# Performance work log

Measured on AMD Instinct MI355X. Metric: run time of the kernel, lower is better.

## Reference

```python
import jax, jax.numpy as jnp
import numpy as np

NUM_HEADS = 4
HEAD_DIM = 64  # out_dim // num_heads = 256 // 4
NEG_SLOPE = 0.2


def setup_inputs() -> dict:
    key = jax.random.key(0)
    k1, k2 = jax.random.split(key)
    h = jax.random.normal(k1, (8, 2048, 256), dtype=jnp.float32)
    # Linear(in_dim, head_dim*num_heads, bias=False): store as [in_dim, out_dim]
    W = jax.random.normal(k2, (256, 256), dtype=jnp.float32) * (1.0 / np.sqrt(256.0))
    return {"h": h, "W": W}


def reference(h, W):
    B, T, _ = h.shape
    # Wh: (B, H, T, D)
    Wh = (h @ W).reshape(B, T, NUM_HEADS, HEAD_DIM).transpose(0, 2, 1, 3)
    scale = 1.0 / (HEAD_DIM ** 0.5)
    # full T x T scores per head, LeakyReLU then softmax over keys
    scores = jnp.einsum('bhtd,bhsd->bhts', Wh, Wh) * scale
    attention = jax.nn.softmax(jax.nn.leaky_relu(scores, negative_slope=NEG_SLOPE), axis=-1)
    h_prime = jnp.einsum('bhts,bhsd->bhtd', attention, Wh)
    # concat=True: (B, T, H*D)
    return h_prime.transpose(0, 2, 1, 3).reshape(B, T, NUM_HEADS * HEAD_DIM)
```

## Files before the change

kernel.cpp:

```cpp
#include <hip/hip_runtime.h>

#define T_SEQ 2048
#define NH 4
#define DH 64

typedef __bf16 bf16x8 __attribute__((ext_vector_type(8)));
typedef float f32x4 __attribute__((ext_vector_type(4)));

__device__ __forceinline__ unsigned short f2bf_rne(float x) {
  unsigned int u = __builtin_bit_cast(unsigned int, x);
  u += 0x7fffu + ((u >> 16) & 1u);
  return (unsigned short)(u >> 16);
}

__device__ __forceinline__ void async_cp16(const unsigned short* g, unsigned short* l) {
  __builtin_amdgcn_global_load_lds(
      (const __attribute__((address_space(1))) unsigned int*)g,
      (__attribute__((address_space(3))) unsigned int*)l, 16, 0, 0);
}

__global__ __launch_bounds__(256, 2) void wh_gemm(
    const float* __restrict__ h, const float* __restrict__ W,
    unsigned short* __restrict__ Kb, unsigned short* __restrict__ Vt) {
  __shared__ __align__(16) float hs[32 * 256];
  const int tid = threadIdx.x;
  const int mbase = blockIdx.x * 32;
  const float4* hblk = (const float4*)(h + (size_t)mbase * 256);
#pragma unroll
  for (int i = 0; i < 8; i++) {
    int slot = i * 256 + tid;
    ((float4*)hs)[slot] = hblk[slot];
  }
  __syncthreads();
  const int nid = tid & 63;
  const int rg = tid >> 6;
  float acc[8][4];
#pragma unroll
  for (int r = 0; r < 8; r++)
#pragma unroll
    for (int j = 0; j < 4; j++) acc[r][j] = 0.f;
  const float4* Wv = (const float4*)W;
  for (int k = 0; k < 256; k += 2) {
    float4 w0 = Wv[k * 64 + nid];
    float4 w1 = Wv[(k + 1) * 64 + nid];
#pragma unroll
    for (int r = 0; r < 8; r++) {
      float2 hv = *(const float2*)&hs[(rg * 8 + r) * 256 + k];
      acc[r][0] += hv.x * w0.x; acc[r][1] += hv.x * w0.y;
      acc[r][2] += hv.x * w0.z; acc[r][3] += hv.x * w0.w;
      acc[r][0] += hv.y * w1.x; acc[r][1] += hv.y * w1.y;
      acc[r][2] += hv.y * w1.z; acc[r][3] += hv.y * w1.w;
    }
  }
  const float s1 = 0.424664717f;
  const int head = nid >> 4;
  const int d0 = (nid & 15) * 4;
#pragma unroll
  for (int r = 0; r < 8; r++) {
    int m = mbase + rg * 8 + r;
    int b = m >> 11, t = m & 2047;
    size_t bh = (size_t)(b * NH + head);
    ushort4 kp;
    kp.x = f2bf_rne(acc[r][0] * s1);
    kp.y = f2bf_rne(acc[r][1] * s1);
    kp.z = f2bf_rne(acc[r][2] * s1);
    kp.w = f2bf_rne(acc[r][3] * s1);
    *(ushort4*)&Kb[(bh * T_SEQ + t) * DH + d0] = kp;
    size_t vtb = (bh * DH + d0) * T_SEQ + t;
    Vt[vtb]             = f2bf_rne(acc[r][0]);
    Vt[vtb + T_SEQ]     = f2bf_rne(acc[r][1]);
    Vt[vtb + 2 * T_SEQ] = f2bf_rne(acc[r][2]);
    Vt[vtb + 3 * T_SEQ] = f2bf_rne(acc[r][3]);
  }
}

__global__ __launch_bounds__(256, 4) void attn(
    const unsigned short* __restrict__ Kb, const unsigned short* __restrict__ Vt,
    float* __restrict__ out) {
  __shared__ __align__(16) unsigned short ldsK[64 * 64];
  __shared__ __align__(16) unsigned short ldsV[64 * 64];
  __shared__ __align__(16) unsigned short ldsP[4][16 * 64];
  const int tid = threadIdx.x;
  const int wave = tid >> 6;
  const int lane = tid & 63;
  const int l15 = lane & 15;
  const int quad = lane >> 4;
  const int bh = blockIdx.x >> 5;
  const int qtile = blockIdx.x & 31;
  const unsigned short* Kbh = Kb + (size_t)bh * T_SEQ * DH;
  const unsigned short* Vbh = Vt + (size_t)bh * DH * T_SEQ;

  const int qrow = qtile * 64 + wave * 16 + l15;
  bf16x8 aq0 = *(const bf16x8*)&Kbh[qrow * DH + quad * 8];
  bf16x8 aq1 = *(const bf16x8*)&Kbh[qrow * DH + 32 + quad * 8];

  f32x4 o[4];
  float lsum[4];
#pragma unroll
  for (int i = 0; i < 4; i++) {
    o[i] = (f32x4){0.f, 0.f, 0.f, 0.f};
    lsum[i] = 0.f;
  }
  unsigned short* Pw = ldsP[wave];

  for (int kt = 0; kt < 32; kt++) {
    __syncthreads();
#pragma unroll
    for (int i = 0; i < 2; i++) {
      int slot = i * 256 + tid;
      int r = slot >> 3;
      int c = (slot & 7) ^ (r & 7);
      unsigned short* lb = &ldsK[(i * 256 + wave * 64) * 8];
      async_cp16(&Kbh[(kt * 64 + r) * DH + c * 8], lb);
      unsigned short* lbv = &ldsV[(i * 256 + wave * 64) * 8];
      async_cp16(&Vbh[(size_t)r * T_SEQ + kt * 64 + c * 8], lbv);
    }
    __syncthreads();

    f32x4 sfr[4];
#pragma unroll
    for (int nt = 0; nt < 4; nt++) {
      int key = nt * 16 + l15;
      bf16x8 kf0 = *(const bf16x8*)&ldsK[key * 64 + ((quad ^ (key & 7)) << 3)];
      bf16x8 kf1 = *(const bf16x8*)&ldsK[key * 64 + (((4 + quad) ^ (key & 7)) << 3)];
      f32x4 s = {0.f, 0.f, 0.f, 0.f};
      s = __builtin_amdgcn_mfma_f32_16x16x32_bf16(aq0, kf0, s, 0, 0, 0);
      s = __builtin_amdgcn_mfma_f32_16x16x32_bf16(aq1, kf1, s, 0, 0, 0);
      sfr[nt] = s;
    }

#pragma unroll
    for (int nt = 0; nt < 4; nt++) {
      int col = nt * 16 + l15;
#pragma unroll
      for (int reg = 0; reg < 4; reg++) {
        float v = sfr[nt][reg];
        float e = __builtin_amdgcn_exp2f(fmaxf(v, 0.2f * v));
        lsum[reg] += e;
        int row = quad * 4 + reg;
        Pw[(row << 6) + (((((col >> 3) ^ (row & 7))) << 3) | (col & 7))] =
            (unsigned short)(__builtin_bit_cast(unsigned int, e) >> 16);
      }
    }
    __builtin_amdgcn_s_waitcnt(0xC07F);

#pragma unroll
    for (int kc = 0; kc < 2; kc++) {
      bf16x8 ap = *(const bf16x8*)&Pw[(l15 << 6) + ((((kc << 2) + quad) ^ (l15 & 7)) << 3)];
#pragma unroll
      for (int nt = 0; nt < 4; nt++) {
        int d = nt * 16 + l15;
        bf16x8 vf = *(const bf16x8*)&ldsV[(d << 6) + ((((kc << 2) + quad) ^ (d & 7)) << 3)];
        o[nt] = __builtin_amdgcn_mfma_f32_16x16x32_bf16(ap, vf, o[nt], 0, 0, 0);
      }
    }
  }

  float inv[4];
#pragma unroll
  for (int reg = 0; reg < 4; reg++) {
    float l = lsum[reg];
    l += __shfl_xor(l, 1, 64);
    l += __shfl_xor(l, 2, 64);
    l += __shfl_xor(l, 4, 64);
    l += __shfl_xor(l, 8, 64);
    inv[reg] = 1.0f / l;
  }
  const int b = bh >> 2, head = bh & 3;
#pragma unroll
  for (int nt = 0; nt < 4; nt++) {
    int d = nt * 16 + l15;
#pragma unroll
    for (int reg = 0; reg < 4; reg++) {
      int trow = qtile * 64 + wave * 16 + quad * 4 + reg;
      out[((size_t)b * T_SEQ + trow) * 256 + head * 64 + d] = o[nt][reg] * inv[reg];
    }
  }
}

extern "C" void kernel_launch(void* const* d_in, const int* in_sizes, int n_in,
                              void* d_out, int out_size, void* d_ws, size_t ws_size,
                              hipStream_t stream) {
  const float* h = (const float*)d_in[0];
  const float* W = (const float*)d_in[1];
  float* out = (float*)d_out;
  unsigned short* Kb = (unsigned short*)d_ws;
  unsigned short* Vt = Kb + (size_t)32 * T_SEQ * DH;
  wh_gemm<<<512, 256, 0, stream>>>(h, W, Kb, Vt);
  attn<<<32 * 32, 256, 0, stream>>>(Kb, Vt, out);
}
```

Baseline: 161.3 us.

## Use split-bf16 MFMA for projection GEMM and double-buffer attention K/V tiles

The fp32 FMA projection GEMM is replaced with bf16 MFMA using a hi/lo split (three MFMAs per tile) to keep near-fp32 accuracy. A new prep kernel transposes W into split bf16 form. The attention kernel now double-buffers K/V LDS tiles with async prefetch of the next tile, raises wave priority around the MFMA sections, and remaps block IDs across XCDs for L2 locality. This adds an extra kernel launch and doubles LDS use, which may reduce occupancy.

```diff
diff --git a/kernel.cpp b/kernel.cpp
--- a/kernel.cpp
+++ b/kernel.cpp
@@ -6,6 +6,7 @@
 
 typedef __bf16 bf16x8 __attribute__((ext_vector_type(8)));
 typedef float f32x4 __attribute__((ext_vector_type(4)));
+typedef unsigned short u16x8 __attribute__((ext_vector_type(8)));
 
 __device__ __forceinline__ unsigned short f2bf_rne(float x) {
   unsigned int u = __builtin_bit_cast(unsigned int, x);
@@ -19,74 +20,107 @@
       (__attribute__((address_space(3))) unsigned int*)l, 16, 0, 0);
 }
 
+__global__ __launch_bounds__(256) void wprep(const float* __restrict__ W,
+                                             unsigned short* __restrict__ Wt) {
+  int tid = blockIdx.x * 256 + threadIdx.x;
+  int k = tid >> 8, n = tid & 255;
+  float w = W[tid];
+  unsigned int u = __builtin_bit_cast(unsigned int, w);
+  unsigned short hi = (unsigned short)(u >> 16);
+  float fhi = __builtin_bit_cast(float, u & 0xffff0000u);
+  float lo = w - fhi;
+  Wt[n * 256 + k] = hi;
+  Wt[65536 + n * 256 + k] =
+      (unsigned short)(__builtin_bit_cast(unsigned int, lo) >> 16);
+}
+
 __global__ __launch_bounds__(256, 2) void wh_gemm(
-    const float* __restrict__ h, const float* __restrict__ W,
+    const float* __restrict__ h, const unsigned short* __restrict__ Wt,
     unsigned short* __restrict__ Kb, unsigned short* __restrict__ Vt) {
-  __shared__ __align__(16) float hs[32 * 256];
   const int tid = threadIdx.x;
+  const int wave = tid >> 6;
+  const int lane = tid & 63;
+  const int l15 = lane & 15;
+  const int quad = lane >> 4;
   const int mbase = blockIdx.x * 32;
-  const float4* hblk = (const float4*)(h + (size_t)mbase * 256);
-#pragma unroll
-  for (int i = 0; i < 8; i++) {
-    int slot = i * 256 + tid;
-    ((float4*)hs)[slot] = hblk[slot];
-  }
-  __syncthreads();
-  const int nid = tid & 63;
-  const int rg = tid >> 6;
-  float acc[8][4];
-#pragma unroll
-  for (int r = 0; r < 8; r++)
-#pragma unroll
-    for (int j = 0; j < 4; j++) acc[r][j] = 0.f;
-  const float4* Wv = (const float4*)W;
-  for (int k = 0; k < 256; k += 2) {
-    float4 w0 = Wv[k * 64 + nid];
-    float4 w1 = Wv[(k + 1) * 64 + nid];
-#pragma unroll
-    for (int r = 0; r < 8; r++) {
-      float2 hv = *(const float2*)&hs[(rg * 8 + r) * 256 + k];
-      acc[r][0] += hv.x * w0.x; acc[r][1] += hv.x * w0.y;
-      acc[r][2] += hv.x * w0.z; acc[r][3] += hv.x * w0.w;
-      acc[r][0] += hv.y * w1.x; acc[r][1] += hv.y * w1.y;
-      acc[r][2] += hv.y * w1.z; acc[r][3] += hv.y * w1.w;
-    }
-  }
+  const int col0 = wave * 64;
+
+  f32x4 acc[2][4];
+#pragma unroll
+  for (int mt = 0; mt < 2; mt++)
+#pragma unroll
+    for (int nt = 0; nt < 4; nt++) acc[mt][nt] = (f32x4){0.f, 0.f, 0.f, 0.f};
+
+  for (int ks = 0; ks < 8; ks++) {
+    const int k0 = ks * 32 + quad * 8;
+    bf16x8 ahi[2], alo[2];
+#pragma unroll
+    for (int mt = 0; mt < 2; mt++) {
+      const float* hp = h + (size_t)(mbase + mt * 16 + l15) * 256 + k0;
+      float xf[8];
+      *(float4*)&xf[0] = *(const float4*)hp;
+      *(float4*)&xf[4] = *(const float4*)(hp + 4);
+      u16x8 hh, ll;
+#pragma unroll
+      for (int j = 0; j < 8; j++) {
+        unsigned int u = __builtin_bit_cast(unsigned int, xf[j]);
+        hh[j] = (unsigned short)(u >> 16);
+        float lo = xf[j] - __builtin_bit_cast(float, u & 0xffff0000u);
+        ll[j] = (unsigned short)(__builtin_bit_cast(unsigned int, lo) >> 16);
+      }
+      ahi[mt] = __builtin_bit_cast(bf16x8, hh);
+      alo[mt] = __builtin_bit_cast(bf16x8, ll);
+    }
+#pragma unroll
+    for (int nt = 0; nt < 4; nt++) {
+      const unsigned short* wp = Wt + ((size_t)(col0 + nt * 16 + l15) << 8) + k0;
+      bf16x8 bhi = *(const bf16x8*)wp;
+      bf16x8 blo = *(const bf16x8*)(wp + 65536);
+#pragma unroll
+      for (int mt = 0; mt < 2; mt++) {
+        acc[mt][nt] = __builtin_amdgcn_mfma_f32_16x16x32_bf16(ahi[mt], bhi, acc[mt][nt], 0, 0, 0);
+        acc[mt][nt] = __builtin_amdgcn_mfma_f32_16x16x32_bf16(alo[mt], bhi, acc[mt][nt], 0, 0, 0);
+        acc[mt][nt] = __builtin_amdgcn_mfma_f32_16x16x32_bf16(ahi[mt], blo, acc[mt][nt], 0, 0, 0);
+      }
+    }
+  }
+
   const float s1 = 0.424664717f;
-  const int head = nid >> 4;
-  const int d0 = (nid & 15) * 4;
-#pragma unroll
-  for (int r = 0; r < 8; r++) {
-    int m = mbase + rg * 8 + r;
-    int b = m >> 11, t = m & 2047;
-    size_t bh = (size_t)(b * NH + head);
-    ushort4 kp;
-    kp.x = f2bf_rne(acc[r][0] * s1);
-    kp.y = f2bf_rne(acc[r][1] * s1);
-    kp.z = f2bf_rne(acc[r][2] * s1);
-    kp.w = f2bf_rne(acc[r][3] * s1);
-    *(ushort4*)&Kb[(bh * T_SEQ + t) * DH + d0] = kp;
-    size_t vtb = (bh * DH + d0) * T_SEQ + t;
-    Vt[vtb]             = f2bf_rne(acc[r][0]);
-    Vt[vtb + T_SEQ]     = f2bf_rne(acc[r][1]);
-    Vt[vtb + 2 * T_SEQ] = f2bf_rne(acc[r][2]);
-    Vt[vtb + 3 * T_SEQ] = f2bf_rne(acc[r][3]);
+#pragma unroll
+  for (int mt = 0; mt < 2; mt++) {
+    int row = mbase + mt * 16 + quad * 4;
+    int b = row >> 11;
+    int tb = row & 2047;
+    size_t bh = (size_t)(b * NH + wave);
+#pragma unroll
+    for (int nt = 0; nt < 4; nt++) {
+      int d = nt * 16 + l15;
+      ushort4 vp;
+#pragma unroll
+      for (int r = 0; r < 4; r++) {
+        float v = acc[mt][nt][r];
+        Kb[(bh * T_SEQ + tb + r) * DH + d] = f2bf_rne(v * s1);
+        ((unsigned short*)&vp)[r] = f2bf_rne(v);
+      }
+      *(ushort4*)&Vt[(bh * DH + d) * T_SEQ + tb] = vp;
+    }
   }
 }
 
 __global__ __launch_bounds__(256, 4) void attn(
     const unsigned short* __restrict__ Kb, const unsigned short* __restrict__ Vt,
     float* __restrict__ out) {
-  __shared__ __align__(16) unsigned short ldsK[64 * 64];
-  __shared__ __align__(16) unsigned short ldsV[64 * 64];
+  __shared__ __align__(16) unsigned short ldsK[2][64 * 64];
+  __shared__ __align__(16) unsigned short ldsV[2][64 * 64];
   __shared__ __align__(16) unsigned short ldsP[4][16 * 64];
   const int tid = threadIdx.x;
   const int wave = tid >> 6;
   const int lane = tid & 63;
   const int l15 = lane & 15;
   const int quad = lane >> 4;
-  const int bh = blockIdx.x >> 5;
-  const int qtile = blockIdx.x & 31;
+  const int lbid = (blockIdx.x & 7) * 128 + (blockIdx.x >> 3);
+  const int bh = lbid >> 5;
+  const int qtile = lbid & 31;
   const unsigned short* Kbh = Kb + (size_t)bh * T_SEQ * DH;
   const unsigned short* Vbh = Vt + (size_t)bh * DH * T_SEQ;
 
@@ -103,31 +137,48 @@
   }
   unsigned short* Pw = ldsP[wave];
 
-  for (int kt = 0; kt < 32; kt++) {
-    __syncthreads();
+  auto stage = [&](int t, int buf) {
 #pragma unroll
     for (int i = 0; i < 2; i++) {
       int slot = i * 256 + tid;
       int r = slot >> 3;
       int c = (slot & 7) ^ (r & 7);
-      unsigned short* lb = &ldsK[(i * 256 + wave * 64) * 8];
-      async_cp16(&Kbh[(kt * 64 + r) * DH + c * 8], lb);
-      unsigned short* lbv = &ldsV[(i * 256 + wave * 64) * 8];
-      async_cp16(&Vbh[(size_t)r * T_SEQ + kt * 64 + c * 8], lbv);
-    }
-    __syncthreads();
+      async_cp16(&Kbh[(t * 64 + r) * DH + c * 8],
+                 &ldsK[buf][(i * 256 + wave * 64) * 8]);
+      async_cp16(&Vbh[(size_t)r * T_SEQ + t * 64 + c * 8],
+                 &ldsV[buf][(i * 256 + wave * 64) * 8]);
+    }
+  };
+
+  stage(0, 0);
+
+  for (int kt = 0; kt < 32; kt++) {
+    const int cur = kt & 1;
+    if (kt < 31) {
+      stage(kt + 1, cur ^ 1);
+      asm volatile("s_waitcnt vmcnt(4)" ::: "memory");
+    } else {
+      asm volatile("s_waitcnt vmcnt(0)" ::: "memory");
+    }
+    __builtin_amdgcn_s_barrier();
+    __builtin_amdgcn_sched_barrier(0);
+
+    const unsigned short* Kl = ldsK[cur];
+    const unsigned short* Vl = ldsV[cur];
 
     f32x4 sfr[4];
+    __builtin_amdgcn_s_setprio(1);
 #pragma unroll
     for (int nt = 0; nt < 4; nt++) {
       int key = nt * 16 + l15;
-      bf16x8 kf0 = *(const bf16x8*)&ldsK[key * 64 + ((quad ^ (key & 7)) << 3)];
-      bf16x8 kf1 = *(const bf16x8*)&ldsK[key * 64 + (((4 + quad) ^ (key & 7)) << 3)];
+      bf16x8 kf0 = *(const bf16x8*)&Kl[key * 64 + ((quad ^ (key & 7)) << 3)];
+      bf16x8 kf1 = *(const bf16x8*)&Kl[key * 64 + (((4 + quad) ^ (key & 7)) << 3)];
       f32x4 s = {0.f, 0.f, 0.f, 0.f};
       s = __builtin_amdgcn_mfma_f32_16x16x32_bf16(aq0, kf0, s, 0, 0, 0);
       s = __builtin_amdgcn_mfma_f32_16x16x32_bf16(aq1, kf1, s, 0, 0, 0);
       sfr[nt] = s;
     }
+    __builtin_amdgcn_s_setprio(0);
 
 #pragma unroll
     for (int nt = 0; nt < 4; nt++) {
@@ -144,16 +195,20 @@
     }
     __builtin_amdgcn_s_waitcnt(0xC07F);
 
+    __builtin_amdgcn_s_setprio(1);
 #pragma unroll
     for (int kc = 0; kc < 2; kc++) {
       bf16x8 ap = *(const bf16x8*)&Pw[(l15 << 6) + ((((kc << 2) + quad) ^ (l15 & 7)) << 3)];
 #pragma unroll
       for (int nt = 0; nt < 4; nt++) {
         int d = nt * 16 + l15;
-        bf16x8 vf = *(const bf16x8*)&ldsV[(d << 6) + ((((kc << 2) + quad) ^ (d & 7)) << 3)];
+        bf16x8 vf = *(const bf16x8*)&Vl[(d << 6) + ((((kc << 2) + quad) ^ (d & 7)) << 3)];
         o[nt] = __builtin_amdgcn_mfma_f32_16x16x32_bf16(ap, vf, o[nt], 0, 0, 0);
       }
     }
+    __builtin_amdgcn_s_setprio(0);
+    __builtin_amdgcn_sched_barrier(0);
+    __builtin_amdgcn_s_barrier();
   }
 
   float inv[4];
@@ -186,6 +241,8 @@
   float* out = (float*)d_out;
   unsigned short* Kb = (unsigned short*)d_ws;
   unsigned short* Vt = Kb + (size_t)32 * T_SEQ * DH;
-  wh_gemm<<<512, 256, 0, stream>>>(h, W, Kb, Vt);
+  unsigned short* Wt = Vt + (size_t)32 * T_SEQ * DH;
+  wprep<<<256, 256, 0, stream>>>(W, Wt);
+  wh_gemm<<<512, 256, 0, stream>>>(h, Wt, Kb, Vt);
   attn<<<32 * 32, 256, 0, stream>>>(Kb, Vt, out);
 }
```

New measurement: 150.5 us. 6.7% less time.
